# Kernel optimization log

Hardware: AMD Instinct MI355X
Metric: run time of the kernel (lower is better)

Reference implementation:

```python
import jax, jax.numpy as jnp
import numpy as np

B, C, H, W = 2, 256, 96, 96
CQ = C // 8  # q/k channel dim = 32


def setup_inputs() -> dict:
    key = jax.random.key(0)
    k1, k2, k3 = jax.random.split(key, 3)
    x = jax.random.normal(k1, (B, C, H, W), dtype=jnp.float32)
    # 1x1 conv weight [out=2*C/8+C, in=C] (spectral_norm is a weight
    # parametrization; post-normalization the forward is a plain 1x1 conv,
    # so we treat w as the already-normalized weight). Scaled ~ unit sigma.
    w = jax.random.normal(k2, (2 * CQ + C, C), dtype=jnp.float32) * 0.05
    gamma = jax.random.normal(k3, (1,), dtype=jnp.float32)
    return {"x": x, "w": w, "gamma": gamma}


def reference(x, w, gamma):
    b, c, h, wd = x.shape
    n = h * wd
    xf = x.reshape(b, c, n)                      # [B, C, N]
    qkv = jnp.einsum('oc,bcn->bon', w, xf)       # 1x1 conv == channel matmul
    q = qkv[:, :CQ]                              # [B, C/8, N]
    k = qkv[:, CQ:2 * CQ]                        # [B, C/8, N]
    v = qkv[:, 2 * CQ:]                          # [B, C,   N]
    scores = jnp.einsum('bdi,bdj->bij', q, k)    # [B, N, N] = q^T k
    attn = jax.nn.softmax(scores, axis=1)        # softmax over i (dim=1)
    o = jnp.einsum('bci,bij->bcj', v, attn)      # [B, C, N]
    return (gamma * o).reshape(b, c, h, wd) + x
```

## Files before the change

kernel.cpp:

```cpp
#include <hip/hip_runtime.h>
#include <hip/hip_bf16.h>

#define NTOK 9216
#define CCH  256
#define DQK  32
#define BJ   128
#define BI   64
#define SSEG 8
#define SI   72

typedef __attribute__((ext_vector_type(8))) short short8;
typedef __attribute__((ext_vector_type(4))) float f32x4;

__device__ __forceinline__ unsigned short f2bf(float x) {
    union { float f; unsigned int u; } v; v.f = x;
    return (unsigned short)((v.u + 0x7FFF + ((v.u >> 16) & 1)) >> 16);
}
__device__ __forceinline__ float bf2f(unsigned short h) {
    union { unsigned int u; float f; } v; v.u = ((unsigned int)h) << 16; return v.f;
}

#if __has_builtin(__builtin_amdgcn_cvt_pk_bf16_f32)
__device__ __forceinline__ unsigned int pack2bf(float a, float b) {
    auto p = __builtin_amdgcn_cvt_pk_bf16_f32(a, b);
    union { decltype(p) v; unsigned int u; } cv; cv.v = p; return cv.u;
}
#else
__device__ __forceinline__ unsigned int pack2bf(float a, float b) {
    return (unsigned)f2bf(a) | ((unsigned)f2bf(b) << 16);
}
#endif

#if __has_builtin(__builtin_amdgcn_exp2f)
#define EXP2(x) __builtin_amdgcn_exp2f(x)
#else
#define EXP2(x) __expf((x) * 0.69314718055994531f)
#endif

__global__ __launch_bounds__(256) void wcvt_kernel(
    const float* __restrict__ w, unsigned short* __restrict__ wbf)
{
    const int i = (blockIdx.x * 256 + threadIdx.x) * 4;
    f32x4 v = *(const f32x4*)(w + i);
    *(unsigned int*)(wbf + i)     = pack2bf(v[0], v[1]);
    *(unsigned int*)(wbf + i + 2) = pack2bf(v[2], v[3]);
}

__global__ __launch_bounds__(256) void qkv_kernel(
    const float* __restrict__ x, const unsigned short* __restrict__ wbf,
    unsigned short* __restrict__ qT, unsigned short* __restrict__ kT,
    unsigned short* __restrict__ vcn)
{
    const int id   = blockIdx.x;
    const int b    = id & 1;
    const int n0   = (id >> 1) * 16;
    const int t    = threadIdx.x;
    const int wv   = t >> 6;
    const int lane = t & 63;
    const int l15  = lane & 15;
    const int qd   = lane >> 4;

    const float* xb = x + (size_t)b * CCH * NTOK + n0 + l15;

    f32x4 acc[5];
#pragma unroll
    for (int tt = 0; tt < 5; ++tt) acc[tt] = (f32x4){0.f, 0.f, 0.f, 0.f};

    const unsigned short* wrow = wbf + (size_t)(80 * wv + l15) * CCH + qd * 8;

#pragma unroll
    for (int kk = 0; kk < 8; ++kk) {
        float xe[8];
#pragma unroll
        for (int e = 0; e < 8; ++e)
            xe[e] = xb[(size_t)(32 * kk + 8 * qd + e) * NTOK];
        short8 bfr;
#pragma unroll
        for (int e = 0; e < 8; ++e)
            bfr[e] = (short)f2bf(xe[e]);
#pragma unroll
        for (int tt = 0; tt < 5; ++tt) {
            short8 afr = *(const short8*)(wrow + (size_t)(16 * tt) * CCH + 32 * kk);
            acc[tt] = __builtin_amdgcn_mfma_f32_16x16x32_bf16(afr, bfr, acc[tt], 0, 0, 0);
        }
    }

    const int n = n0 + l15;
    const float L2E = 1.44269504088896f;
#pragma unroll
    for (int tt = 0; tt < 5; ++tt) {
        const int o0l = 80 * wv + 16 * tt + 4 * qd;
        if (o0l < 32) {
            unsigned short* d = qT + ((size_t)b * NTOK + n) * DQK + o0l;
            *(unsigned int*)d       = pack2bf(acc[tt][0] * L2E, acc[tt][1] * L2E);
            *(unsigned int*)(d + 2) = pack2bf(acc[tt][2] * L2E, acc[tt][3] * L2E);
        } else if (o0l < 64) {
            unsigned short* d = kT + ((size_t)b * NTOK + n) * DQK + (o0l - 32);
            *(unsigned int*)d       = pack2bf(acc[tt][0], acc[tt][1]);
            *(unsigned int*)(d + 2) = pack2bf(acc[tt][2], acc[tt][3]);
        } else {
            unsigned short* d = vcn + ((size_t)b * CCH + (o0l - 64)) * NTOK + n;
            d[0] = f2bf(acc[tt][0]);
            d[(size_t)NTOK] = f2bf(acc[tt][1]);
            d[(size_t)2 * NTOK] = f2bf(acc[tt][2]);
            d[(size_t)3 * NTOK] = f2bf(acc[tt][3]);
        }
    }
}

__global__ __launch_bounds__(256, 3) void attn_partial_kernel(
    const unsigned short* __restrict__ qT, const unsigned short* __restrict__ kT,
    const unsigned short* __restrict__ vcn,
    unsigned short* __restrict__ Opart, float* __restrict__ lpart)
{
    __shared__ __align__(16) unsigned short Pl[BJ * SI];
    __shared__ float lred2[2 * BJ];

    const int id    = blockIdx.x;
    const int combo = id & 15;
    const int s     = combo >> 1;
    const int cb    = combo & 1;
    const int r     = id >> 4;
    const int jb    = r % 72;
    const int b     = r / 72;

    const int t    = threadIdx.x;
    const int wv   = t >> 6;
    const int lane = t & 63;
    const int l15  = lane & 15;
    const int qd   = lane >> 4;
    const int jh   = wv >> 1;
    const int u    = wv & 1;
    const int j0   = jb * BJ;
    const int c0   = cb * 128;
    const int iBeg = s * (NTOK / SSEG);
    const int iEnd = iBeg + (NTOK / SSEG);

    short8 kf[4];
#pragma unroll
    for (int jt = 0; jt < 4; ++jt)
        kf[jt] = *(const short8*)(kT +
            ((size_t)b * NTOK + j0 + 64 * jh + 16 * jt + l15) * DQK + qd * 8);

    f32x4 acc[4][4];
#pragma unroll
    for (int mt = 0; mt < 4; ++mt)
#pragma unroll
        for (int ct = 0; ct < 4; ++ct)
            acc[mt][ct] = (f32x4){0.f, 0.f, 0.f, 0.f};
    float lw[4] = {0.f, 0.f, 0.f, 0.f};

    const unsigned short* qrow =
        qT + (size_t)b * NTOK * DQK + (size_t)(16 * u + l15) * DQK + qd * 8;
    const unsigned short* vrow =
        vcn + ((size_t)b * CCH + c0 + 64 * u + l15) * NTOK + qd * 8;

    for (int i0 = iBeg; i0 < iEnd; i0 += BI) {
        short8 af[2];
#pragma unroll
        for (int it = 0; it < 2; ++it)
            af[it] = *(const short8*)(qrow + (size_t)(i0 + 32 * it) * DQK);
        short8 vf[2][4];
#pragma unroll
        for (int kc = 0; kc < 2; ++kc)
#pragma unroll
            for (int ct = 0; ct < 4; ++ct)
                vf[kc][ct] = *(const short8*)(vrow + (size_t)(16 * ct) * NTOK + i0 + 32 * kc);

#pragma unroll
        for (int it = 0; it < 2; ++it) {
#pragma unroll
            for (int jt = 0; jt < 4; ++jt) {
                f32x4 sc = __builtin_amdgcn_mfma_f32_16x16x32_bf16(
                    af[it], kf[jt], (f32x4){0.f, 0.f, 0.f, 0.f}, 0, 0, 0);
                float p0 = EXP2(sc[0]);
                float p1 = EXP2(sc[1]);
                float p2 = EXP2(sc[2]);
                float p3 = EXP2(sc[3]);
                lw[jt] += (p0 + p1) + (p2 + p3);
                int base = (64 * jh + 16 * jt + l15) * SI + 32 * it + 16 * u + 4 * qd;
                *(unsigned long long*)(Pl + base) =
                    (unsigned long long)pack2bf(p0, p1) |
                    ((unsigned long long)pack2bf(p2, p3) << 32);
            }
        }
        __syncthreads();

#pragma unroll
        for (int kc = 0; kc < 2; ++kc) {
            short8 pa[4];
#pragma unroll
            for (int mt = 0; mt < 4; ++mt)
                pa[mt] = *(const short8*)(Pl + (64 * jh + 16 * mt + l15) * SI + 32 * kc + qd * 8);
#pragma unroll
            for (int mt = 0; mt < 4; ++mt)
#pragma unroll
                for (int ct = 0; ct < 4; ++ct)
                    acc[mt][ct] = __builtin_amdgcn_mfma_f32_16x16x32_bf16(
                        pa[mt], vf[kc][ct], acc[mt][ct], 0, 0, 0);
        }
        __syncthreads();
    }

#pragma unroll
    for (int jt = 0; jt < 4; ++jt) {
        lw[jt] += __shfl_xor(lw[jt], 16);
        lw[jt] += __shfl_xor(lw[jt], 32);
    }
    if (qd == 0) {
#pragma unroll
        for (int jt = 0; jt < 4; ++jt)
            lred2[u * BJ + 64 * jh + 16 * jt + l15] = lw[jt];
    }
    __syncthreads();
    if (cb == 0 && t < BJ)
        lpart[(size_t)(s * 2 + b) * NTOK + j0 + t] = lred2[t] + lred2[BJ + t];

#pragma unroll
    for (int mt = 0; mt < 4; ++mt)
#pragma unroll
        for (int ct = 0; ct < 4; ++ct) {
            int c = c0 + 64 * u + 16 * ct + l15;
            int j = j0 + 64 * jh + 16 * mt + 4 * qd;
            unsigned short* p = Opart + ((size_t)(s * 2 + b) * CCH + c) * NTOK + j;
            *(unsigned long long*)p =
                (unsigned long long)pack2bf(acc[mt][ct][0], acc[mt][ct][1]) |
                ((unsigned long long)pack2bf(acc[mt][ct][2], acc[mt][ct][3]) << 32);
        }
}

__global__ __launch_bounds__(256) void reduce_kernel(
    const unsigned short* __restrict__ Opart, const float* __restrict__ lpart,
    const float* __restrict__ x, const float* __restrict__ gamma,
    float* __restrict__ out)
{
    const size_t flat = ((size_t)blockIdx.x * 256 + threadIdx.x) * 4;
    const int j = (int)(flat % NTOK);
    const int b = (int)(flat / ((size_t)CCH * NTOK));
    const size_t inb = flat - (size_t)b * CCH * NTOK;

    f32x4 o = {0.f, 0.f, 0.f, 0.f};
    f32x4 l = {0.f, 0.f, 0.f, 0.f};
#pragma unroll
    for (int s = 0; s < SSEG; ++s) {
        const size_t plane = (size_t)(s * 2 + b) * CCH * NTOK;
        unsigned long long ov = *(const unsigned long long*)(Opart + plane + inb);
        f32x4 lv = *(const f32x4*)(lpart + (size_t)(s * 2 + b) * NTOK + j);
        o[0] += bf2f((unsigned short)(ov));
        o[1] += bf2f((unsigned short)(ov >> 16));
        o[2] += bf2f((unsigned short)(ov >> 32));
        o[3] += bf2f((unsigned short)(ov >> 48));
        l[0] += lv[0]; l[1] += lv[1]; l[2] += lv[2]; l[3] += lv[3];
    }
    const float g = gamma[0];
    f32x4 xv = *(const f32x4*)(x + flat);
    f32x4 rr;
    rr[0] = g * o[0] / l[0] + xv[0];
    rr[1] = g * o[1] / l[1] + xv[1];
    rr[2] = g * o[2] / l[2] + xv[2];
    rr[3] = g * o[3] / l[3] + xv[3];
    *(f32x4*)(out + flat) = rr;
}

extern "C" void kernel_launch(void* const* d_in, const int* in_sizes, int n_in,
                              void* d_out, int out_size, void* d_ws, size_t ws_size,
                              hipStream_t stream) {
    const float* x     = (const float*)d_in[0];
    const float* w     = (const float*)d_in[1];
    const float* gamma = (const float*)d_in[2];
    float* out = (float*)d_out;

    unsigned short* qT  = (unsigned short*)d_ws;
    unsigned short* kT  = qT + (size_t)2 * NTOK * DQK;
    unsigned short* vcn = kT + (size_t)2 * NTOK * DQK;
    unsigned short* Opart = vcn + (size_t)2 * CCH * NTOK;
    float* lpart = (float*)(Opart + (size_t)SSEG * 2 * CCH * NTOK);
    unsigned short* wbf = (unsigned short*)(lpart + (size_t)SSEG * 2 * NTOK);

    wcvt_kernel<<<80, 256, 0, stream>>>(w, wbf);

    qkv_kernel<<<1152, 256, 0, stream>>>(x, wbf, qT, kT, vcn);

    attn_partial_kernel<<<2304, 256, 0, stream>>>(qT, kT, vcn, Opart, lpart);

    reduce_kernel<<<(unsigned)((size_t)2 * CCH * NTOK / 4 / 256), 256, 0, stream>>>(
        Opart, lpart, x, gamma, out);
}
```

Before: 299.2 us.

## Keep softmax probabilities in registers using 32x32 MFMA and lane shuffles

Rewrites the attention partial kernel so that each wave owns 32 key columns and computes scores with 32x32x16 bf16 MFMA. The exponentiated probabilities are rearranged between lane halves with xor-32 shuffles so they can feed the P·V MFMA directly as an operand. This removes the shared-memory staging buffer and both block barriers per iteration. In exchange, each wave now loads its own V and Q fragments with no sharing between waves, and the output store becomes scalar 2-byte writes instead of 8-byte vector stores.

```diff
diff --git a/kernel.cpp b/kernel.cpp
--- a/kernel.cpp
+++ b/kernel.cpp
@@ -5,12 +5,11 @@
 #define CCH  256
 #define DQK  32
 #define BJ   128
-#define BI   64
 #define SSEG 8
-#define SI   72
 
 typedef __attribute__((ext_vector_type(8))) short short8;
 typedef __attribute__((ext_vector_type(4))) float f32x4;
+typedef __attribute__((ext_vector_type(16))) float f32x16;
 
 __device__ __forceinline__ unsigned short f2bf(float x) {
     union { float f; unsigned int u; } v; v.f = x;
@@ -36,6 +35,13 @@
 #else
 #define EXP2(x) __expf((x) * 0.69314718055994531f)
 #endif
+
+__device__ __forceinline__ f32x16 zero16() {
+    f32x16 z;
+#pragma unroll
+    for (int i = 0; i < 16; ++i) z[i] = 0.f;
+    return z;
+}
 
 __global__ __launch_bounds__(256) void wcvt_kernel(
     const float* __restrict__ w, unsigned short* __restrict__ wbf)
@@ -113,9 +119,6 @@
     const unsigned short* __restrict__ vcn,
     unsigned short* __restrict__ Opart, float* __restrict__ lpart)
 {
-    __shared__ __align__(16) unsigned short Pl[BJ * SI];
-    __shared__ float lred2[2 * BJ];
-
     const int id    = blockIdx.x;
     const int combo = id & 15;
     const int s     = combo >> 1;
@@ -127,105 +130,85 @@
     const int t    = threadIdx.x;
     const int wv   = t >> 6;
     const int lane = t & 63;
-    const int l15  = lane & 15;
-    const int qd   = lane >> 4;
-    const int jh   = wv >> 1;
-    const int u    = wv & 1;
-    const int j0   = jb * BJ;
+    const int l31  = lane & 31;
+    const int b5   = lane >> 5;
+    const int jw   = jb * BJ + 32 * wv;
     const int c0   = cb * 128;
     const int iBeg = s * (NTOK / SSEG);
     const int iEnd = iBeg + (NTOK / SSEG);
 
-    short8 kf[4];
-#pragma unroll
-    for (int jt = 0; jt < 4; ++jt)
-        kf[jt] = *(const short8*)(kT +
-            ((size_t)b * NTOK + j0 + 64 * jh + 16 * jt + l15) * DQK + qd * 8);
-
-    f32x4 acc[4][4];
-#pragma unroll
-    for (int mt = 0; mt < 4; ++mt)
-#pragma unroll
-        for (int ct = 0; ct < 4; ++ct)
-            acc[mt][ct] = (f32x4){0.f, 0.f, 0.f, 0.f};
-    float lw[4] = {0.f, 0.f, 0.f, 0.f};
-
-    const unsigned short* qrow =
-        qT + (size_t)b * NTOK * DQK + (size_t)(16 * u + l15) * DQK + qd * 8;
-    const unsigned short* vrow =
-        vcn + ((size_t)b * CCH + c0 + 64 * u + l15) * NTOK + qd * 8;
-
-    for (int i0 = iBeg; i0 < iEnd; i0 += BI) {
-        short8 af[2];
-#pragma unroll
-        for (int it = 0; it < 2; ++it)
-            af[it] = *(const short8*)(qrow + (size_t)(i0 + 32 * it) * DQK);
-        short8 vf[2][4];
-#pragma unroll
-        for (int kc = 0; kc < 2; ++kc)
-#pragma unroll
-            for (int ct = 0; ct < 4; ++ct)
-                vf[kc][ct] = *(const short8*)(vrow + (size_t)(16 * ct) * NTOK + i0 + 32 * kc);
-
+    short8 kf[2];
+#pragma unroll
+    for (int kd = 0; kd < 2; ++kd)
+        kf[kd] = *(const short8*)(kT + ((size_t)b * NTOK + jw + l31) * DQK + 16 * kd + 8 * b5);
+
+    f32x16 acc[4];
+#pragma unroll
+    for (int ct = 0; ct < 4; ++ct) acc[ct] = zero16();
+    float lw = 0.f;
+
+    const unsigned short* qbase = qT + ((size_t)b * NTOK + l31) * DQK + 8 * b5;
+    const unsigned short* vbase = vcn + ((size_t)b * CCH + c0 + l31) * NTOK + 8 * b5;
+
+#pragma unroll 1
+    for (int i0 = iBeg; i0 < iEnd; i0 += 64) {
 #pragma unroll
         for (int it = 0; it < 2; ++it) {
-#pragma unroll
-            for (int jt = 0; jt < 4; ++jt) {
-                f32x4 sc = __builtin_amdgcn_mfma_f32_16x16x32_bf16(
-                    af[it], kf[jt], (f32x4){0.f, 0.f, 0.f, 0.f}, 0, 0, 0);
-                float p0 = EXP2(sc[0]);
-                float p1 = EXP2(sc[1]);
-                float p2 = EXP2(sc[2]);
-                float p3 = EXP2(sc[3]);
-                lw[jt] += (p0 + p1) + (p2 + p3);
-                int base = (64 * jh + 16 * jt + l15) * SI + 32 * it + 16 * u + 4 * qd;
-                *(unsigned long long*)(Pl + base) =
-                    (unsigned long long)pack2bf(p0, p1) |
-                    ((unsigned long long)pack2bf(p2, p3) << 32);
+            const int ib = i0 + 32 * it;
+            short8 vf[2][4];
+#pragma unroll
+            for (int kc2 = 0; kc2 < 2; ++kc2)
+#pragma unroll
+                for (int ct = 0; ct < 4; ++ct)
+                    vf[kc2][ct] = *(const short8*)(vbase + (size_t)(32 * ct) * NTOK + ib + 16 * kc2);
+
+            short8 af0 = *(const short8*)(qbase + (size_t)ib * DQK);
+            short8 af1 = *(const short8*)(qbase + (size_t)ib * DQK + 16);
+            f32x16 sc = __builtin_amdgcn_mfma_f32_32x32x16_bf16(af0, kf[0], zero16(), 0, 0, 0);
+            sc = __builtin_amdgcn_mfma_f32_32x32x16_bf16(af1, kf[1], sc, 0, 0, 0);
+
+            unsigned int pk[8];
+            float ls = 0.f;
+#pragma unroll
+            for (int w = 0; w < 8; ++w) {
+                float p0 = EXP2(sc[2 * w]);
+                float p1 = EXP2(sc[2 * w + 1]);
+                ls += p0 + p1;
+                pk[w] = pack2bf(p0, p1);
             }
-        }
-        __syncthreads();
-
-#pragma unroll
-        for (int kc = 0; kc < 2; ++kc) {
-            short8 pa[4];
-#pragma unroll
-            for (int mt = 0; mt < 4; ++mt)
-                pa[mt] = *(const short8*)(Pl + (64 * jh + 16 * mt + l15) * SI + 32 * kc + qd * 8);
-#pragma unroll
-            for (int mt = 0; mt < 4; ++mt)
+            lw += ls;
+
+#pragma unroll
+            for (int kc2 = 0; kc2 < 2; ++kc2) {
+                const int base = 4 * kc2;
+                unsigned int m1 = b5 ? pk[base]     : pk[base + 2];
+                unsigned int m2 = b5 ? pk[base + 1] : pk[base + 3];
+                unsigned int x1 = __shfl_xor(m1, 32);
+                unsigned int x2 = __shfl_xor(m2, 32);
+                unsigned int wd0 = b5 ? x1 : pk[base];
+                unsigned int wd1 = b5 ? x2 : pk[base + 1];
+                unsigned int wd2 = b5 ? pk[base + 2] : x1;
+                unsigned int wd3 = b5 ? pk[base + 3] : x2;
+                union { unsigned int u[4]; short8 s8; } bu;
+                bu.u[0] = wd0; bu.u[1] = wd1; bu.u[2] = wd2; bu.u[3] = wd3;
 #pragma unroll
                 for (int ct = 0; ct < 4; ++ct)
-                    acc[mt][ct] = __builtin_amdgcn_mfma_f32_16x16x32_bf16(
-                        pa[mt], vf[kc][ct], acc[mt][ct], 0, 0, 0);
-        }
-        __syncthreads();
-    }
-
-#pragma unroll
-    for (int jt = 0; jt < 4; ++jt) {
-        lw[jt] += __shfl_xor(lw[jt], 16);
-        lw[jt] += __shfl_xor(lw[jt], 32);
-    }
-    if (qd == 0) {
-#pragma unroll
-        for (int jt = 0; jt < 4; ++jt)
-            lred2[u * BJ + 64 * jh + 16 * jt + l15] = lw[jt];
-    }
-    __syncthreads();
-    if (cb == 0 && t < BJ)
-        lpart[(size_t)(s * 2 + b) * NTOK + j0 + t] = lred2[t] + lred2[BJ + t];
-
-#pragma unroll
-    for (int mt = 0; mt < 4; ++mt)
-#pragma unroll
-        for (int ct = 0; ct < 4; ++ct) {
-            int c = c0 + 64 * u + 16 * ct + l15;
-            int j = j0 + 64 * jh + 16 * mt + 4 * qd;
-            unsigned short* p = Opart + ((size_t)(s * 2 + b) * CCH + c) * NTOK + j;
-            *(unsigned long long*)p =
-                (unsigned long long)pack2bf(acc[mt][ct][0], acc[mt][ct][1]) |
-                ((unsigned long long)pack2bf(acc[mt][ct][2], acc[mt][ct][3]) << 32);
+                    acc[ct] = __builtin_amdgcn_mfma_f32_32x32x16_bf16(
+                        vf[kc2][ct], bu.s8, acc[ct], 0, 0, 0);
+            }
+        }
+    }
+
+    float lt = lw + __shfl_xor(lw, 32);
+    if (cb == 0 && lane < 32)
+        lpart[(size_t)(s * 2 + b) * NTOK + jw + l31] = lt;
+
+#pragma unroll
+    for (int ct = 0; ct < 4; ++ct)
+#pragma unroll
+        for (int w = 0; w < 16; ++w) {
+            const int c = c0 + 32 * ct + (w & 3) + 8 * (w >> 2) + 4 * b5;
+            Opart[((size_t)(s * 2 + b) * CCH + c) * NTOK + jw + l31] = f2bf(acc[ct][w]);
         }
 }
 
```

Measured after the change: 445.6 us. 48.9% more time.
